# Kernel tuning notes

Measured on AMD Instinct MI355X. Metric: run time of the kernel, lower is better.

## Reference

```python
import math
import jax, jax.numpy as jnp
import numpy as np

B, S, DIM = 1, 1024, 2048
H, KVH, HD = 16, 4, 128
HID, L, VOCAB = 8192, 2, 32000
NIMG, TOK_START = 256, 1
IMG_IN = 2 * 14 * 14 * 3  # temporal_patch*spatial_patch^2*channels
EPS = 1e-6


def _rms(x, w=None, eps=EPS):
    y = x * jax.lax.rsqrt(jnp.mean(x * x, axis=-1, keepdims=True) + eps)
    return y if w is None else y * w


def _rope(x, angles):
    # x: [B,S,H,D], angles: [S, D//2] pairwise rotation angles (3D RoPE: 1D+2D concat)
    c = jnp.cos(angles)[None, :, None, :]
    s = jnp.sin(angles)[None, :, None, :]
    x1, x2 = x[..., 0::2], x[..., 1::2]
    return jnp.stack([x1 * c - x2 * s, x1 * s + x2 * c], axis=-1).reshape(x.shape)


def setup_inputs() -> dict:
    key = jax.random.key(0)
    ks = jax.random.split(key, 12)
    sc = 0.02
    return {
        "tokens": jax.random.randint(ks[0], (B, S), 0, VOCAB),
        "img_feats": jax.random.normal(ks[1], (B, NIMG, IMG_IN), jnp.float32),
        "freqs_cis": jax.random.normal(ks[2], (S, HD // 4), jnp.float32),
        "freqs_cis_2d": jax.random.normal(ks[3], (S, HD // 4), jnp.float32),
        "tok_emb": jax.random.normal(ks[4], (VOCAB, DIM), jnp.float32) * sc,
        "img_proj_w": jax.random.normal(ks[5], (DIM, IMG_IN), jnp.float32) * sc,
        "wqkv": jax.random.normal(ks[6], (L, H * HD + 2 * KVH * HD, DIM), jnp.float32) * sc,
        "wo": jax.random.normal(ks[7], (L, DIM, H * HD), jnp.float32) * sc,
        "sinks": jax.random.normal(ks[8], (L, H), jnp.float32),
        "w13": jax.random.normal(ks[9], (L, 2 * HID, DIM), jnp.float32) * sc,
        "w2": jax.random.normal(ks[10], (L, DIM, HID), jnp.float32) * sc,
        "norm_w": jnp.ones((DIM,), jnp.float32),
        "output_w": jax.random.normal(ks[11], (VOCAB, DIM), jnp.float32) * sc,
    }


def reference(tokens, img_feats, freqs_cis, freqs_cis_2d, tok_emb, img_proj_w,
              wqkv, wo, sinks, w13, w2, norm_w, output_w):
    # token embeddings + slice-based scatter of projected image tokens
    x = tok_emb[tokens]                                   # [B,S,DIM]
    img = jnp.einsum('bnf,df->bnd', img_feats, img_proj_w)
    x = jax.lax.dynamic_update_slice(x, img, (0, TOK_START, 0))

    angles = jnp.concatenate([freqs_cis, freqs_cis_2d], axis=-1)  # [S, HD//2]
    scale = 1.0 / math.sqrt(HD)
    neg = jnp.where(jnp.tril(jnp.ones((S, S), bool)), 0.0, -jnp.inf)  # causal
    n_rep = H // KVH
    q_dim, kv_dim = H * HD, KVH * HD

    for i in range(L):
        # attention: RMSNorm -> QKV -> QK-norm -> GQA expand -> RoPE -> SDPA+lse
        h = _rms(x)
        qkv = h @ wqkv[i].T
        q = qkv[..., :q_dim].reshape(B, S, H, HD)
        k = qkv[..., q_dim:q_dim + kv_dim].reshape(B, S, KVH, HD)
        v = qkv[..., q_dim + kv_dim:].reshape(B, S, KVH, HD)
        q, k = _rms(q), _rms(k)
        k = jnp.repeat(k, n_rep, axis=2)  # repeat_interleave over kv heads
        v = jnp.repeat(v, n_rep, axis=2)
        q, k = _rope(q, angles), _rope(k, angles)
        scores = jnp.einsum('bqhd,bkhd->bhqk', q, k) * scale + neg
        lse = jax.nn.logsumexp(scores, axis=-1)            # [B,H,S]
        attn = jnp.exp(scores - lse[..., None])
        out = jnp.einsum('bhqk,bkhd->bqhd', attn, v)        # [B,S,H,HD]
        sink_scale = jax.nn.sigmoid(lse - sinks[i][None, :, None])  # [B,H,S]
        out = out * sink_scale.transpose(0, 2, 1)[..., None]
        x = x + out.reshape(B, S, H * HD) @ wo[i].T

        # FFN: RMSNorm -> interleaved gate/up -> relu(gate)^2 * up -> down
        h = _rms(x)
        packed = h @ w13[i].T
        gate, up = packed[..., 0::2], packed[..., 1::2]
        x = x + (jnp.square(jax.nn.relu(gate)) * up) @ w2[i].T

    return _rms(x, norm_w) @ output_w.T                    # [B,S,VOCAB]
```

## Files before the change

kernel.cpp:

```cpp
#include <hip/hip_runtime.h>

typedef __bf16 bf16;
typedef bf16 bf16x8 __attribute__((ext_vector_type(8)));
typedef bf16 bf16x4 __attribute__((ext_vector_type(4)));
typedef bf16 bf16x2 __attribute__((ext_vector_type(2)));
typedef float f32x4 __attribute__((ext_vector_type(4)));
typedef float f32x2 __attribute__((ext_vector_type(2)));

#define S_LEN 1024
#define DIM 2048
#define NH 16
#define NKVH 4
#define HD 128
#define HID 8192
#define VOCAB 32000
#define QKV_N 3072
#define W13_N 16384
#define IMG_K 1176
#define NIMG 256

#define AS1 __attribute__((address_space(1)))
#define AS3 __attribute__((address_space(3)))

__device__ inline f32x4 mfma16(bf16x8 a, bf16x8 b, f32x4 c) {
  return __builtin_amdgcn_mfma_f32_16x16x32_bf16(a, b, c, 0, 0, 0);
}

__global__ void embed_kernel(const int* __restrict__ tok, const float* __restrict__ emb,
                             float* __restrict__ x) {
  int s = blockIdx.x, t = threadIdx.x;
  int id = tok[s];
  const float* er = emb + (size_t)id * DIM;
  float* xr = x + (size_t)s * DIM;
  *(f32x4*)(xr + t * 8)     = *(const f32x4*)(er + t * 8);
  *(f32x4*)(xr + t * 8 + 4) = *(const f32x4*)(er + t * 8 + 4);
}

__global__ void cvt_kernel(const float* __restrict__ in, bf16* __restrict__ o, int n) {
  int i = blockIdx.x * 256 + threadIdx.x;
  if (i < n) o[i] = (bf16)in[i];
}
__global__ void cvt4_kernel(const float* __restrict__ in, bf16* __restrict__ o, int n4) {
  int i = blockIdx.x * 256 + threadIdx.x;
  if (i < n4) {
    f32x4 v = *(const f32x4*)(in + (size_t)i * 4);
    bf16x4 b;
    b[0] = (bf16)v[0]; b[1] = (bf16)v[1]; b[2] = (bf16)v[2]; b[3] = (bf16)v[3];
    *(bf16x4*)(o + (size_t)i * 4) = b;
  }
}

template<int USE_W>
__global__ void rmsnorm_kernel(const float* __restrict__ x, const float* __restrict__ w,
                               bf16* __restrict__ o) {
  const int row = blockIdx.x, t = threadIdx.x;
  const float* xr = x + (size_t)row * DIM;
  f32x4 a = *(const f32x4*)(xr + t * 8);
  f32x4 b = *(const f32x4*)(xr + t * 8 + 4);
  float ss = a[0]*a[0] + a[1]*a[1] + a[2]*a[2] + a[3]*a[3]
           + b[0]*b[0] + b[1]*b[1] + b[2]*b[2] + b[3]*b[3];
#pragma unroll
  for (int off = 1; off < 64; off <<= 1) ss += __shfl_xor(ss, off);
  __shared__ float red[4];
  if ((t & 63) == 0) red[t >> 6] = ss;
  __syncthreads();
  ss = red[0] + red[1] + red[2] + red[3];
  float r = rsqrtf(ss * (1.0f / DIM) + 1e-6f);
  bf16x8 ov;
  if (USE_W) {
    f32x4 w1 = *(const f32x4*)(w + t * 8);
    f32x4 w2v = *(const f32x4*)(w + t * 8 + 4);
    ov[0] = (bf16)(a[0]*r*w1[0]); ov[1] = (bf16)(a[1]*r*w1[1]);
    ov[2] = (bf16)(a[2]*r*w1[2]); ov[3] = (bf16)(a[3]*r*w1[3]);
    ov[4] = (bf16)(b[0]*r*w2v[0]); ov[5] = (bf16)(b[1]*r*w2v[1]);
    ov[6] = (bf16)(b[2]*r*w2v[2]); ov[7] = (bf16)(b[3]*r*w2v[3]);
  } else {
    ov[0] = (bf16)(a[0]*r); ov[1] = (bf16)(a[1]*r);
    ov[2] = (bf16)(a[2]*r); ov[3] = (bf16)(a[3]*r);
    ov[4] = (bf16)(b[0]*r); ov[5] = (bf16)(b[1]*r);
    ov[6] = (bf16)(b[2]*r); ov[7] = (bf16)(b[3]*r);
  }
  *(bf16x8*)(o + (size_t)row * DIM + t * 8) = ov;
}

__global__ void qkvpost_kernel(const float* __restrict__ qkv, const float* __restrict__ f1,
                               const float* __restrict__ f2, bf16* __restrict__ qb,
                               bf16* __restrict__ kb, bf16* __restrict__ vtb) {
  int s = blockIdx.x, t = threadIdx.x;
  __shared__ float cs[64], sn[64];
  if (t < 64) {
    float ang = (t < 32) ? f1[(size_t)s * 32 + t] : f2[(size_t)s * 32 + (t - 32)];
    cs[t] = cosf(ang);
    sn[t] = sinf(ang);
  }
  __syncthreads();
  int w = t >> 6, lane = t & 63;
  for (int hh = w; hh < 24; hh += 4) {
    const float* base = qkv + (size_t)s * QKV_N + hh * HD;
    f32x2 e = *(const f32x2*)(base + lane * 2);
    if (hh < 20) {
      float ssum = e[0]*e[0] + e[1]*e[1];
#pragma unroll
      for (int off = 1; off < 64; off <<= 1) ssum += __shfl_xor(ssum, off);
      float r = rsqrtf(ssum * (1.0f / HD) + 1e-6f);
      float x1 = e[0] * r, x2 = e[1] * r;
      float c = cs[lane], s2 = sn[lane];
      bf16x2 ov;
      ov[0] = (bf16)(x1 * c - x2 * s2);
      ov[1] = (bf16)(x1 * s2 + x2 * c);
      if (hh < 16)
        *(bf16x2*)(qb + ((size_t)hh * S_LEN + s) * HD + lane * 2) = ov;
      else
        *(bf16x2*)(kb + ((size_t)(hh - 16) * S_LEN + s) * HD + lane * 2) = ov;
    } else {
      int kv = hh - 20;
      vtb[((size_t)kv * HD + lane * 2) * S_LEN + s]     = (bf16)e[0];
      vtb[((size_t)kv * HD + lane * 2 + 1) * S_LEN + s] = (bf16)e[1];
    }
  }
}

__global__ __launch_bounds__(256) void attn_kernel(const bf16* __restrict__ qb,
                                                   const bf16* __restrict__ kb,
                                                   const bf16* __restrict__ vtb,
                                                   const float* __restrict__ sinks,
                                                   bf16* __restrict__ out) {
  const int h = blockIdx.y, qs = blockIdx.x;
  const int w = threadIdx.x >> 6, lane = threadIdx.x & 63;
  const int lo = lane & 15, hi = lane >> 4;
  const int q0 = qs * 16;
  const int q = q0 + lo;
  const int kvh = h >> 2;
  const bf16* Q = qb + (size_t)h * S_LEN * HD;
  const bf16* Kp = kb + (size_t)kvh * S_LEN * HD;
  const bf16* Vt = vtb + (size_t)kvh * HD * S_LEN;
  const float scale = 0.08838834764831845f;

  __shared__ float accS[4][64 * 36];
  __shared__ float mS[4][16], lS[4][16];

  bf16x8 qf[4];
#pragma unroll
  for (int ks = 0; ks < 4; ++ks)
    qf[ks] = *(const bf16x8*)(Q + (size_t)q * HD + ks * 32 + hi * 8);

  f32x4 accT[8];
#pragma unroll
  for (int i = 0; i < 8; ++i) accT[i] = (f32x4){0.f, 0.f, 0.f, 0.f};
  float mrow = -3e38f, lrow = 0.f;

  const int ntc = (q0 + 15) / 64 + 1;
  for (int c = w; c < ntc; c += 4) {
    const int kv0 = c * 64;
    f32x4 st[4];
#pragma unroll
    for (int f = 0; f < 4; ++f) st[f] = (f32x4){0.f, 0.f, 0.f, 0.f};
#pragma unroll
    for (int ks = 0; ks < 4; ++ks) {
      const bf16* kbase = Kp + (size_t)(kv0 + lo) * HD + ks * 32 + hi * 8;
#pragma unroll
      for (int f = 0; f < 4; ++f) {
        bf16x8 kf = *(const bf16x8*)(kbase + (size_t)f * 16 * HD);
        st[f] = mfma16(kf, qf[ks], st[f]);
      }
    }
    float p[4][4];
    float pmax = -3e38f;
#pragma unroll
    for (int f = 0; f < 4; ++f)
#pragma unroll
      for (int r = 0; r < 4; ++r) {
        int kvg = kv0 + f * 16 + hi * 4 + r;
        float v = (kvg <= q) ? st[f][r] * scale : -3e38f;
        p[f][r] = v;
        pmax = fmaxf(pmax, v);
      }
    pmax = fmaxf(pmax, __shfl_xor(pmax, 16));
    pmax = fmaxf(pmax, __shfl_xor(pmax, 32));
    float mnew = fmaxf(mrow, pmax);
    float alpha = __expf(mrow - mnew);
    float ps = 0.f;
#pragma unroll
    for (int f = 0; f < 4; ++f)
#pragma unroll
      for (int r = 0; r < 4; ++r) {
        float e = __expf(p[f][r] - mnew);
        p[f][r] = e;
        ps += e;
      }
    ps += __shfl_xor(ps, 16);
    ps += __shfl_xor(ps, 32);
    lrow = lrow * alpha + ps;
    mrow = mnew;
#pragma unroll
    for (int fd = 0; fd < 8; ++fd) {
      accT[fd][0] *= alpha; accT[fd][1] *= alpha;
      accT[fd][2] *= alpha; accT[fd][3] *= alpha;
    }
    bf16x8 pb0, pb1;
#pragma unroll
    for (int j = 0; j < 8; ++j) {
      int src = ((j >> 2) + 2 * (hi & 1)) * 16 + lo;
      float v0 = __shfl(p[0][j & 3], src);
      float v1 = __shfl(p[1][j & 3], src);
      pb0[j] = (bf16)((hi >= 2) ? v1 : v0);
      float v2 = __shfl(p[2][j & 3], src);
      float v3 = __shfl(p[3][j & 3], src);
      pb1[j] = (bf16)((hi >= 2) ? v3 : v2);
    }
#pragma unroll
    for (int fd = 0; fd < 8; ++fd) {
      const bf16* vrow = Vt + (size_t)(fd * 16 + lo) * S_LEN + kv0 + hi * 8;
      bf16x8 vf0 = *(const bf16x8*)(vrow);
      bf16x8 vf1 = *(const bf16x8*)(vrow + 32);
      accT[fd] = mfma16(vf0, pb0, accT[fd]);
      accT[fd] = mfma16(vf1, pb1, accT[fd]);
    }
  }
  if (hi == 0) { mS[w][lo] = mrow; lS[w][lo] = lrow; }
  float* as = &accS[w][lane * 36];
#pragma unroll
  for (int fd = 0; fd < 8; ++fd) *(f32x4*)(as + fd * 4) = accT[fd];
  __syncthreads();
  float m0 = mS[0][lo], m1 = mS[1][lo], m2 = mS[2][lo], m3 = mS[3][lo];
  float mstar = fmaxf(fmaxf(m0, m1), fmaxf(m2, m3));
  float e0 = __expf(m0 - mstar), e1 = __expf(m1 - mstar);
  float e2 = __expf(m2 - mstar), e3 = __expf(m3 - mstar);
  float lstar = lS[0][lo]*e0 + lS[1][lo]*e1 + lS[2][lo]*e2 + lS[3][lo]*e3;
  float lse = mstar + __logf(lstar);
  float ssig = 1.f / (1.f + __expf(sinks[h] - lse));
  float sc = ssig / lstar;
#pragma unroll
  for (int f2 = 0; f2 < 2; ++f2) {
    int fd = w * 2 + f2;
    f32x4 a0 = *(const f32x4*)&accS[0][lane * 36 + fd * 4];
    f32x4 a1 = *(const f32x4*)&accS[1][lane * 36 + fd * 4];
    f32x4 a2 = *(const f32x4*)&accS[2][lane * 36 + fd * 4];
    f32x4 a3 = *(const f32x4*)&accS[3][lane * 36 + fd * 4];
#pragma unroll
    for (int r = 0; r < 4; ++r) {
      float o = a0[r]*e0 + a1[r]*e1 + a2[r]*e2 + a3[r]*e3;
      out[(size_t)q * DIM + h * HD + fd * 16 + hi * 4 + r] = (bf16)(o * sc);
    }
  }
}

__device__ inline void xcd_remap(int ntm, int ntn, int& mtile, int& ntile) {
  const int flat = blockIdx.x + ntm * blockIdx.y;
  const int chunk = ntm * 8;
  const int gfull = ntn >> 3;
  const int g = flat / chunk;
  if (g < gfull) {
    int rem = flat - g * chunk;
    ntile = g * 8 + (rem & 7);
    mtile = rem >> 3;
  } else {
    int rem = flat - gfull * chunk;
    int nrem = ntn - gfull * 8;
    ntile = gfull * 8 + rem % nrem;
    mtile = rem / nrem;
  }
}

enum { EPI_STORE = 0, EPI_ADD = 1, EPI_ACT = 2, EPI_ADDA = 3 };

template<int BM, int BN, int EPI, int GL>
__global__ void gemm_bt(const bf16* __restrict__ A, const float* __restrict__ W,
                        float* __restrict__ C, bf16* __restrict__ Cb,
                        int M, int N, int K, int ldc) {
  constexpr int BK = 64;
  __shared__ __align__(16) char lds[(BM + BN) * BK * 2];
  char* ldsA = lds;
  char* ldsB = lds + BM * BK * 2;
  const int t = threadIdx.x;
  int mtile, ntile;
  xcd_remap(gridDim.x, gridDim.y, mtile, ntile);
  const int m0 = mtile * BM, n0 = ntile * BN;

  const int wid = t >> 6, lane = t & 63;
  const int lo = lane & 15, hi = lane >> 4;
  const int wr = wid >> 1, wc = wid & 1;
  constexpr int TM = BM / 32, TN = BN / 32;
  constexpr int NA = BM / 32;
  constexpr int NPASS = BM / 32;
  constexpr int NW = BN / 16;

  f32x4 acc[TM][TN];
#pragma unroll
  for (int m = 0; m < TM; ++m)
#pragma unroll
    for (int n = 0; n < TN; ++n) acc[m][n] = (f32x4){0.f, 0.f, 0.f, 0.f};

  const int nk = (K + BK - 1) / BK;
  for (int kt = 0; kt < nk; ++kt) {
    const int k0 = kt * BK;
    bf16x8 av[NA];
    f32x4 wv[NW];
    if (!GL) {
#pragma unroll
      for (int i = 0; i < NA; ++i) {
        int c = t + i * 256;
        int row = c >> 3, kc = c & 7;
        int kg = k0 + kc * 8;
        bf16x8 z = {};
        av[i] = (kg < K) ? *(const bf16x8*)(A + (size_t)(m0 + row) * K + kg) : z;
      }
    }
#pragma unroll
    for (int i = 0; i < NW; ++i) {
      int c = t + i * 256;
      int row = c >> 4, kc = c & 15;
      int kg = k0 + kc * 4;
      f32x4 z = (f32x4){0.f, 0.f, 0.f, 0.f};
      wv[i] = (kg < K) ? *(const f32x4*)(W + (size_t)(n0 + row) * K + kg) : z;
    }
    __syncthreads();
    if (GL) {
#pragma unroll
      for (int i = 0; i < NPASS; ++i) {
        int row = i * 32 + (t >> 3);
        int srcb = ((t & 7) * 16) ^ ((row & 7) << 4);
        const bf16* g2 = A + (size_t)(m0 + row) * K + k0 + (srcb >> 1);
        char* l = ldsA + i * 4096 + wid * 1024;
        __builtin_amdgcn_global_load_lds((const AS1 void*)g2, (AS3 void*)l, 16, 0, 0);
      }
    } else {
#pragma unroll
      for (int i = 0; i < NA; ++i) {
        int c = t + i * 256;
        int row = c >> 3, kc = c & 7;
        int kb = (kc * 16) ^ ((row & 7) << 4);
        *(bf16x8*)(ldsA + row * 128 + kb) = av[i];
      }
    }
#pragma unroll
    for (int i = 0; i < NW; ++i) {
      int c = t + i * 256;
      int row = c >> 4, kc = c & 15;
      bf16x4 bv;
      bv[0] = (bf16)wv[i][0]; bv[1] = (bf16)wv[i][1];
      bv[2] = (bf16)wv[i][2]; bv[3] = (bf16)wv[i][3];
      int kb = (kc * 8) ^ ((row & 7) << 4);
      *(bf16x4*)(ldsB + row * 128 + kb) = bv;
    }
    __syncthreads();
#pragma unroll
    for (int ks = 0; ks < 2; ++ks) {
      bf16x8 af[TM], bfr[TN];
      int kbb = ks * 64 + hi * 16;
#pragma unroll
      for (int m = 0; m < TM; ++m) {
        int row = wr * (BM / 2) + m * 16 + lo;
        af[m] = *(const bf16x8*)(ldsA + row * 128 + (kbb ^ ((row & 7) << 4)));
      }
#pragma unroll
      for (int n = 0; n < TN; ++n) {
        int row = wc * (BN / 2) + n * 16 + lo;
        bfr[n] = *(const bf16x8*)(ldsB + row * 128 + (kbb ^ ((row & 7) << 4)));
      }
#pragma unroll
      for (int m = 0; m < TM; ++m)
#pragma unroll
        for (int n = 0; n < TN; ++n)
          acc[m][n] = mfma16(af[m], bfr[n], acc[m][n]);
    }
    __syncthreads();
  }
#pragma unroll
  for (int m = 0; m < TM; ++m) {
    int gmb = m0 + wr * (BM / 2) + m * 16 + hi * 4;
#pragma unroll
    for (int n = 0; n < TN; ++n) {
      int gn = n0 + wc * (BN / 2) + n * 16 + lo;
#pragma unroll
      for (int r = 0; r < 4; ++r) {
        float v = acc[m][n][r];
        if (EPI == EPI_STORE) {
          C[(size_t)(gmb + r) * ldc + gn] = v;
        } else if (EPI == EPI_ADD) {
          C[(size_t)(gmb + r) * ldc + gn] += v;
        } else {
          float pv = __shfl_xor(v, 1);
          if (!(lane & 1)) {
            float g2 = fmaxf(v, 0.f);
            Cb[(size_t)(gmb + r) * (W13_N / 2) + (gn >> 1)] = (bf16)(g2 * g2 * pv);
          }
        }
      }
    }
  }
}

template<int BM, int BN, int EPI>
__global__ __launch_bounds__(256) void gemm_bb(const bf16* __restrict__ A,
                                               const bf16* __restrict__ W,
                                               float* __restrict__ C, bf16* __restrict__ Cb,
                                               int strideK, int kLen, int ldc) {
  constexpr int BK = 64;
  __shared__ __align__(16) char lds[(BM + BN) * BK * 2];
  char* ldsA = lds;
  char* ldsB = lds + BM * BK * 2;
  const int t = threadIdx.x;
  int mtile, ntile;
  xcd_remap(gridDim.x, gridDim.y, mtile, ntile);
  const int m0 = mtile * BM, n0 = ntile * BN;
  const int koff = blockIdx.z * kLen;

  const int wid = t >> 6, lane = t & 63;
  const int lo = lane & 15, hi = lane >> 4;
  const int wr = wid >> 1, wc = wid & 1;
  constexpr int TM = BM / 32, TN = BN / 32;
  constexpr int PA = BM / 32, PB = BN / 32;

  f32x4 acc[TM][TN];
#pragma unroll
  for (int m = 0; m < TM; ++m)
#pragma unroll
    for (int n = 0; n < TN; ++n) acc[m][n] = (f32x4){0.f, 0.f, 0.f, 0.f};

  const int prow = t >> 3;
  const int psrcb = (t & 7) * 16;
  const int nk = kLen / BK;
  for (int kt = 0; kt < nk; ++kt) {
    const int k0 = koff + kt * BK;
#pragma unroll
    for (int i = 0; i < PA; ++i) {
      int row = i * 32 + prow;
      int srcb = psrcb ^ ((row & 7) << 4);
      const bf16* g = A + (size_t)(m0 + row) * strideK + k0 + (srcb >> 1);
      __builtin_amdgcn_global_load_lds((const AS1 void*)g,
                                       (AS3 void*)(ldsA + i * 4096 + wid * 1024), 16, 0, 0);
    }
#pragma unroll
    for (int i = 0; i < PB; ++i) {
      int row = i * 32 + prow;
      int srcb = psrcb ^ ((row & 7) << 4);
      const bf16* g = W + (size_t)(n0 + row) * strideK + k0 + (srcb >> 1);
      __builtin_amdgcn_global_load_lds((const AS1 void*)g,
                                       (AS3 void*)(ldsB + i * 4096 + wid * 1024), 16, 0, 0);
    }
    __syncthreads();
#pragma unroll
    for (int ks = 0; ks < 2; ++ks) {
      bf16x8 af[TM], bfr[TN];
      int kbb = ks * 64 + hi * 16;
#pragma unroll
      for (int m = 0; m < TM; ++m) {
        int row = wr * (BM / 2) + m * 16 + lo;
        af[m] = *(const bf16x8*)(ldsA + row * 128 + (kbb ^ ((row & 7) << 4)));
      }
#pragma unroll
      for (int n = 0; n < TN; ++n) {
        int row = wc * (BN / 2) + n * 16 + lo;
        bfr[n] = *(const bf16x8*)(ldsB + row * 128 + (kbb ^ ((row & 7) << 4)));
      }
#pragma unroll
      for (int m = 0; m < TM; ++m)
#pragma unroll
        for (int n = 0; n < TN; ++n)
          acc[m][n] = mfma16(af[m], bfr[n], acc[m][n]);
    }
    __syncthreads();
  }
#pragma unroll
  for (int m = 0; m < TM; ++m) {
    int gmb = m0 + wr * (BM / 2) + m * 16 + hi * 4;
#pragma unroll
    for (int n = 0; n < TN; ++n) {
      int gn = n0 + wc * (BN / 2) + n * 16 + lo;
#pragma unroll
      for (int r = 0; r < 4; ++r) {
        float v = acc[m][n][r];
        if (EPI == EPI_STORE) {
          C[(size_t)(gmb + r) * ldc + gn] = v;
        } else if (EPI == EPI_ADD) {
          C[(size_t)(gmb + r) * ldc + gn] += v;
        } else if (EPI == EPI_ADDA) {
          atomicAdd(&C[(size_t)(gmb + r) * ldc + gn], v);
        } else {
          float pv = __shfl_xor(v, 1);
          if (!(lane & 1)) {
            float g2 = fmaxf(v, 0.f);
            Cb[(size_t)(gmb + r) * (W13_N / 2) + (gn >> 1)] = (bf16)(g2 * g2 * pv);
          }
        }
      }
    }
  }
}

template<int EPI>
__global__ __launch_bounds__(512, 1) void gemm_2pf(const bf16* __restrict__ A,
                                                   const float* __restrict__ W,
                                                   float* __restrict__ C, bf16* __restrict__ Cb,
                                                   int K, int ldc) {
  extern __shared__ __align__(16) char lds[];
  char* ldsA = lds;
  char* ldsB = lds + 65536;
  const int t = threadIdx.x;
  int mtile, ntile;
  xcd_remap(gridDim.x, gridDim.y, mtile, ntile);
  const int m0 = mtile * 256, n0 = ntile * 256;
  const int wid = t >> 6, lane = t & 63;
  const int lo = lane & 15, hi = lane >> 4;
  const int wr = wid >> 2, wc = wid & 3;

  f32x4 acc[8][4];
#pragma unroll
  for (int f = 0; f < 8; ++f)
#pragma unroll
    for (int g = 0; g < 4; ++g) acc[f][g] = (f32x4){0.f, 0.f, 0.f, 0.f};

  const int prow = t >> 3;
  const int pcol = (t & 7) * 16;

  auto STAGEA = [&](int h, int kt2) {
    char* dst = ldsA + (kt2 & 1) * 32768 + h * 16384;
    const int k0 = kt2 * 64;
#pragma unroll
    for (int i = 0; i < 2; ++i) {
      int row = i * 64 + prow;
      int srcb = pcol ^ ((row & 7) << 4);
      const bf16* g = A + (size_t)(m0 + h * 128 + row) * K + k0 + (srcb >> 1);
      __builtin_amdgcn_global_load_lds((const AS1 void*)g,
          (AS3 void*)(dst + i * 8192 + wid * 1024), 16, 0, 0);
    }
  };

  f32x4 breg[4][2];
  auto BLOAD = [&](int kt2) {
#pragma unroll
    for (int i = 0; i < 4; ++i) {
      int c = t + i * 512;
      int row = c >> 3, kc = c & 7;
      const float* g = W + (size_t)(n0 + row) * K + kt2 * 64 + kc * 8;
      breg[i][0] = *(const f32x4*)(g);
      breg[i][1] = *(const f32x4*)(g + 4);
    }
  };
  auto BWRITE = [&](int kt2) {
#pragma unroll
    for (int i = 0; i < 4; ++i) {
      int c = t + i * 512;
      int row = c >> 3, kc = c & 7;
      int h = row >> 7, rowh = row & 127;
      bf16x8 bv;
#pragma unroll
      for (int e = 0; e < 4; ++e) {
        bv[e]     = (bf16)breg[i][0][e];
        bv[4 + e] = (bf16)breg[i][1][e];
      }
      *(bf16x8*)(ldsB + (kt2 & 1) * 32768 + h * 16384 + rowh * 128 +
                 ((kc * 16) ^ ((rowh & 7) << 4))) = bv;
    }
  };

  auto LDA = [&](int buf, int mh, int i, int ks) -> bf16x8 {
    int row = (mh * 4 + i) * 16 + lo;
    return *(const bf16x8*)(ldsA + buf * 32768 + wr * 16384 + row * 128 +
                            ((ks * 64 + hi * 16) ^ ((row & 7) << 4)));
  };
  auto LDB = [&](int buf, int nh, int j, int ks) -> bf16x8 {
    int rowh = (wc & 1) * 64 + (nh * 2 + j) * 16 + lo;
    return *(const bf16x8*)(ldsB + buf * 32768 + (wc >> 1) * 16384 + rowh * 128 +
                            ((ks * 64 + hi * 16) ^ ((rowh & 7) << 4)));
  };

  const int nk = K / 64;
  STAGEA(0, 0);
  STAGEA(1, 0);
  __builtin_amdgcn_sched_barrier(0);
  BLOAD(0);
  __builtin_amdgcn_sched_barrier(0);
  asm volatile("s_waitcnt vmcnt(8)" ::: "memory");
  __builtin_amdgcn_s_barrier();
  asm volatile("" ::: "memory");

  for (int kt = 0; kt < nk; ++kt) {
    const int buf = kt & 1;
    const bool more = (kt + 1) < nk;
    BWRITE(kt);
    asm volatile("s_waitcnt lgkmcnt(0)" ::: "memory");
    __builtin_amdgcn_s_barrier();
    asm volatile("" ::: "memory");
    if (more) {
      STAGEA(0, kt + 1);
      STAGEA(1, kt + 1);
      __builtin_amdgcn_sched_barrier(0);
      BLOAD(kt + 1);
      __builtin_amdgcn_sched_barrier(0);
    }
#pragma unroll
    for (int mh = 0; mh < 2; ++mh) {
      bf16x8 a[4][2];
#pragma unroll
      for (int i = 0; i < 4; ++i) { a[i][0] = LDA(buf, mh, i, 0); a[i][1] = LDA(buf, mh, i, 1); }
#pragma unroll
      for (int nh = 0; nh < 2; ++nh) {
        bf16x8 b[2][2];
#pragma unroll
        for (int j = 0; j < 2; ++j) { b[j][0] = LDB(buf, nh, j, 0); b[j][1] = LDB(buf, nh, j, 1); }
        __builtin_amdgcn_s_setprio(1);
#pragma unroll
        for (int i = 0; i < 4; ++i)
#pragma unroll
          for (int j = 0; j < 2; ++j) {
            acc[mh * 4 + i][nh * 2 + j] = mfma16(a[i][0], b[j][0], acc[mh * 4 + i][nh * 2 + j]);
            acc[mh * 4 + i][nh * 2 + j] = mfma16(a[i][1], b[j][1], acc[mh * 4 + i][nh * 2 + j]);
          }
        __builtin_amdgcn_s_setprio(0);
      }
    }
    if (more) asm volatile("s_waitcnt vmcnt(8)" ::: "memory");
    else      asm volatile("s_waitcnt vmcnt(0)" ::: "memory");
    __builtin_amdgcn_s_barrier();
    asm volatile("" ::: "memory");
  }
#pragma unroll
  for (int f = 0; f < 8; ++f) {
    int gmb = m0 + wr * 128 + f * 16 + hi * 4;
#pragma unroll
    for (int g = 0; g < 4; ++g) {
      int gn = n0 + wc * 64 + g * 16 + lo;
#pragma unroll
      for (int r = 0; r < 4; ++r) {
        float v = acc[f][g][r];
        if (EPI == EPI_STORE) {
          C[(size_t)(gmb + r) * ldc + gn] = v;
        } else if (EPI == EPI_ADD) {
          C[(size_t)(gmb + r) * ldc + gn] += v;
        } else {
          float pv = __shfl_xor(v, 1);
          if (!(lane & 1)) {
            float g2 = fmaxf(v, 0.f);
            Cb[(size_t)(gmb + r) * (W13_N / 2) + (gn >> 1)] = (bf16)(g2 * g2 * pv);
          }
        }
      }
    }
  }
}

extern "C" void kernel_launch(void* const* d_in, const int* in_sizes, int n_in,
                              void* d_out, int out_size, void* d_ws, size_t ws_size,
                              hipStream_t stream) {
  const int* tokens = (const int*)d_in[0];
  const float* img_feats = (const float*)d_in[1];
  const float* freqs = (const float*)d_in[2];
  const float* freqs2 = (const float*)d_in[3];
  const float* tok_emb = (const float*)d_in[4];
  const float* img_proj_w = (const float*)d_in[5];
  const float* wqkv = (const float*)d_in[6];
  const float* wo = (const float*)d_in[7];
  const float* sinks = (const float*)d_in[8];
  const float* w13 = (const float*)d_in[9];
  const float* w2 = (const float*)d_in[10];
  const float* norm_w = (const float*)d_in[11];
  const float* output_w = (const float*)d_in[12];
  float* out = (float*)d_out;

  char* ws = (char*)d_ws;
  float* x = (float*)ws;   ws += (size_t)S_LEN * DIM * 4;
  bf16* h = (bf16*)ws;     ws += (size_t)S_LEN * DIM * 2;
  float* qkv = (float*)ws; ws += (size_t)S_LEN * QKV_N * 4;
  bf16* qb = (bf16*)ws;    ws += (size_t)NH * S_LEN * HD * 2;
  bf16* kb = (bf16*)ws;    ws += (size_t)NKVH * S_LEN * HD * 2;
  bf16* vtb = (bf16*)ws;   ws += (size_t)NKVH * HD * S_LEN * 2;
  bf16* ao = (bf16*)ws;    ws += (size_t)S_LEN * DIM * 2;
  bf16* act = (bf16*)ws;   ws += (size_t)S_LEN * HID * 2;
  bf16* imgb = (bf16*)ws;  ws += (size_t)NIMG * IMG_K * 2;
  const size_t n_wqkv = (size_t)2 * QKV_N * DIM;
  const size_t n_wo   = (size_t)2 * DIM * (NH * HD);
  const size_t n_w2   = (size_t)2 * DIM * HID;
  bf16* wqkvb = (bf16*)ws; ws += n_wqkv * 2;
  bf16* wob   = (bf16*)ws; ws += n_wo * 2;
  bf16* w2b   = (bf16*)ws; ws += n_w2 * 2;
  const bool bf16_path = ((size_t)(ws - (char*)d_ws) <= ws_size);

  bool big_ok = false;
  {
    hipError_t e1 = hipFuncSetAttribute((const void*)&gemm_2pf<EPI_STORE>,
                                        hipFuncAttributeMaxDynamicSharedMemorySize, 131072);
    hipError_t e2 = hipFuncSetAttribute((const void*)&gemm_2pf<EPI_ACT>,
                                        hipFuncAttributeMaxDynamicSharedMemorySize, 131072);
    if (e1 == hipSuccess && e2 == hipSuccess) {
      hipFuncAttributes fa1{}, fa2{};
      if (hipFuncGetAttributes(&fa1, (const void*)&gemm_2pf<EPI_STORE>) == hipSuccess &&
          hipFuncGetAttributes(&fa2, (const void*)&gemm_2pf<EPI_ACT>) == hipSuccess)
        big_ok = fa1.maxDynamicSharedSizeBytes >= 131072 &&
                 fa2.maxDynamicSharedSizeBytes >= 131072;
    }
  }

  embed_kernel<<<S_LEN, 256, 0, stream>>>(tokens, tok_emb, x);
  cvt_kernel<<<(NIMG * IMG_K + 255) / 256, 256, 0, stream>>>(img_feats, imgb, NIMG * IMG_K);
  gemm_bt<64, 128, EPI_STORE, 0><<<dim3(NIMG / 64, DIM / 128), 256, 0, stream>>>(
      imgb, img_proj_w, x + DIM, nullptr, NIMG, DIM, IMG_K, DIM);

  if (bf16_path) {
    cvt4_kernel<<<(int)(n_wqkv / 4 + 255) / 256, 256, 0, stream>>>(wqkv, wqkvb, (int)(n_wqkv / 4));
    cvt4_kernel<<<(int)(n_wo / 4 + 255) / 256, 256, 0, stream>>>(wo, wob, (int)(n_wo / 4));
    cvt4_kernel<<<(int)(n_w2 / 4 + 255) / 256, 256, 0, stream>>>(w2, w2b, (int)(n_w2 / 4));
  }

  for (int i = 0; i < 2; ++i) {
    rmsnorm_kernel<0><<<S_LEN, 256, 0, stream>>>(x, nullptr, h);
    if (bf16_path) {
      gemm_bb<64, 128, EPI_STORE><<<dim3(S_LEN / 64, QKV_N / 128, 1), 256, 0, stream>>>(
          h, wqkvb + (size_t)i * QKV_N * DIM, qkv, nullptr, DIM, DIM, QKV_N);
    } else {
      gemm_bt<64, 128, EPI_STORE, 1><<<dim3(S_LEN / 64, QKV_N / 128), 256, 0, stream>>>(
          h, wqkv + (size_t)i * QKV_N * DIM, qkv, nullptr, S_LEN, QKV_N, DIM, QKV_N);
    }
    qkvpost_kernel<<<S_LEN, 256, 0, stream>>>(qkv, freqs, freqs2, qb, kb, vtb);
    attn_kernel<<<dim3(S_LEN / 16, NH), 256, 0, stream>>>(qb, kb, vtb, sinks + i * NH, ao);
    if (bf16_path) {
      gemm_bb<64, 128, EPI_ADDA><<<dim3(S_LEN / 64, DIM / 128, 2), 256, 0, stream>>>(
          ao, wob + (size_t)i * DIM * DIM, x, nullptr, DIM, DIM / 2, DIM);
    } else {
      gemm_bt<64, 128, EPI_ADD, 1><<<dim3(S_LEN / 64, DIM / 128), 256, 0, stream>>>(
          ao, wo + (size_t)i * DIM * DIM, x, nullptr, S_LEN, DIM, DIM, DIM);
    }
    rmsnorm_kernel<0><<<S_LEN, 256, 0, stream>>>(x, nullptr, h);
    if (big_ok) {
      gemm_2pf<EPI_ACT><<<dim3(S_LEN / 256, W13_N / 256), 512, 131072, stream>>>(
          h, w13 + (size_t)i * W13_N * DIM, nullptr, act, DIM, 0);
    } else {
      gemm_bt<128, 128, EPI_ACT, 1><<<dim3(S_LEN / 128, W13_N / 128), 256, 0, stream>>>(
          h, w13 + (size_t)i * W13_N * DIM, nullptr, act, S_LEN, W13_N, DIM, 0);
    }
    if (bf16_path) {
      gemm_bb<64, 128, EPI_ADDA><<<dim3(S_LEN / 64, DIM / 128, 2), 256, 0, stream>>>(
          act, w2b + (size_t)i * DIM * HID, x, nullptr, HID, HID / 2, DIM);
    } else {
      gemm_bt<64, 128, EPI_ADD, 1><<<dim3(S_LEN / 64, DIM / 128), 256, 0, stream>>>(
          act, w2 + (size_t)i * DIM * HID, x, nullptr, S_LEN, DIM, HID, DIM);
    }
  }
  rmsnorm_kernel<1><<<S_LEN, 256, 0, stream>>>(x, norm_w, h);
  if (big_ok) {
    gemm_2pf<EPI_STORE><<<dim3(S_LEN / 256, VOCAB / 256), 512, 131072, stream>>>(
        h, output_w, out, nullptr, DIM, VOCAB);
  } else {
    gemm_bt<128, 128, EPI_STORE, 1><<<dim3(S_LEN / 128, VOCAB / 128), 256, 0, stream>>>(
        h, output_w, out, nullptr, S_LEN, VOCAB, DIM, VOCAB);
  }
}
```

Before: 894.5 us.

## Load fp32 B fragments directly from global into registers, drop B LDS staging

In the 256x256 gemm_2pf kernel, the B (fp32 weight) tile is no longer loaded into registers, converted, and written to LDS. Each wave now reads its own B fragments straight from global memory, converts them to bf16 in registers, and feeds them to MFMA. This halves dynamic LDS to 64KB and removes one barrier plus the LDS write/read traffic per k-step. In exchange, B loads are no longer prefetched a step ahead and are now on the critical path with a vmcnt(0) wait each iteration. Waves that share columns also reload the same B data, raising global/L2 traffic.

```diff
diff --git a/kernel.cpp b/kernel.cpp
--- a/kernel.cpp
+++ b/kernel.cpp
@@ -496,7 +496,6 @@
                                                    int K, int ldc) {
   extern __shared__ __align__(16) char lds[];
   char* ldsA = lds;
-  char* ldsB = lds + 65536;
   const int t = threadIdx.x;
   int mtile, ntile;
   xcd_remap(gridDim.x, gridDim.y, mtile, ntile);
@@ -527,92 +526,62 @@
     }
   };
 
-  f32x4 breg[4][2];
-  auto BLOAD = [&](int kt2) {
-#pragma unroll
-    for (int i = 0; i < 4; ++i) {
-      int c = t + i * 512;
-      int row = c >> 3, kc = c & 7;
-      const float* g = W + (size_t)(n0 + row) * K + kt2 * 64 + kc * 8;
-      breg[i][0] = *(const f32x4*)(g);
-      breg[i][1] = *(const f32x4*)(g + 4);
-    }
-  };
-  auto BWRITE = [&](int kt2) {
-#pragma unroll
-    for (int i = 0; i < 4; ++i) {
-      int c = t + i * 512;
-      int row = c >> 3, kc = c & 7;
-      int h = row >> 7, rowh = row & 127;
-      bf16x8 bv;
-#pragma unroll
-      for (int e = 0; e < 4; ++e) {
-        bv[e]     = (bf16)breg[i][0][e];
-        bv[4 + e] = (bf16)breg[i][1][e];
-      }
-      *(bf16x8*)(ldsB + (kt2 & 1) * 32768 + h * 16384 + rowh * 128 +
-                 ((kc * 16) ^ ((rowh & 7) << 4))) = bv;
-    }
-  };
-
   auto LDA = [&](int buf, int mh, int i, int ks) -> bf16x8 {
     int row = (mh * 4 + i) * 16 + lo;
     return *(const bf16x8*)(ldsA + buf * 32768 + wr * 16384 + row * 128 +
                             ((ks * 64 + hi * 16) ^ ((row & 7) << 4)));
   };
-  auto LDB = [&](int buf, int nh, int j, int ks) -> bf16x8 {
-    int rowh = (wc & 1) * 64 + (nh * 2 + j) * 16 + lo;
-    return *(const bf16x8*)(ldsB + buf * 32768 + (wc >> 1) * 16384 + rowh * 128 +
-                            ((ks * 64 + hi * 16) ^ ((rowh & 7) << 4)));
+  const int bn_base = n0 + (wc >> 1) * 128 + (wc & 1) * 64;
+  auto BFRAG = [&](int nh, int j, int ks, int kt2) -> bf16x8 {
+    const float* g = W + (size_t)(bn_base + (nh * 2 + j) * 16 + lo) * K +
+                     kt2 * 64 + ks * 32 + hi * 8;
+    f32x4 v0 = *(const f32x4*)(g);
+    f32x4 v1 = *(const f32x4*)(g + 4);
+    bf16x8 b;
+#pragma unroll
+    for (int e = 0; e < 4; ++e) { b[e] = (bf16)v0[e]; b[4 + e] = (bf16)v1[e]; }
+    return b;
   };
 
   const int nk = K / 64;
   STAGEA(0, 0);
   STAGEA(1, 0);
-  __builtin_amdgcn_sched_barrier(0);
-  BLOAD(0);
-  __builtin_amdgcn_sched_barrier(0);
-  asm volatile("s_waitcnt vmcnt(8)" ::: "memory");
+  asm volatile("s_waitcnt vmcnt(0)" ::: "memory");
   __builtin_amdgcn_s_barrier();
   asm volatile("" ::: "memory");
 
   for (int kt = 0; kt < nk; ++kt) {
     const int buf = kt & 1;
     const bool more = (kt + 1) < nk;
-    BWRITE(kt);
-    asm volatile("s_waitcnt lgkmcnt(0)" ::: "memory");
-    __builtin_amdgcn_s_barrier();
-    asm volatile("" ::: "memory");
     if (more) {
       STAGEA(0, kt + 1);
       STAGEA(1, kt + 1);
       __builtin_amdgcn_sched_barrier(0);
-      BLOAD(kt + 1);
-      __builtin_amdgcn_sched_barrier(0);
-    }
+    }
+    bf16x8 b00 = BFRAG(0, 0, 0, kt), b01 = BFRAG(0, 0, 1, kt);
+    bf16x8 b10 = BFRAG(0, 1, 0, kt), b11 = BFRAG(0, 1, 1, kt);
+    bf16x8 b20 = BFRAG(1, 0, 0, kt), b21 = BFRAG(1, 0, 1, kt);
+    bf16x8 b30 = BFRAG(1, 1, 0, kt), b31 = BFRAG(1, 1, 1, kt);
 #pragma unroll
     for (int mh = 0; mh < 2; ++mh) {
       bf16x8 a[4][2];
 #pragma unroll
       for (int i = 0; i < 4; ++i) { a[i][0] = LDA(buf, mh, i, 0); a[i][1] = LDA(buf, mh, i, 1); }
-#pragma unroll
-      for (int nh = 0; nh < 2; ++nh) {
-        bf16x8 b[2][2];
-#pragma unroll
-        for (int j = 0; j < 2; ++j) { b[j][0] = LDB(buf, nh, j, 0); b[j][1] = LDB(buf, nh, j, 1); }
-        __builtin_amdgcn_s_setprio(1);
-#pragma unroll
-        for (int i = 0; i < 4; ++i)
-#pragma unroll
-          for (int j = 0; j < 2; ++j) {
-            acc[mh * 4 + i][nh * 2 + j] = mfma16(a[i][0], b[j][0], acc[mh * 4 + i][nh * 2 + j]);
-            acc[mh * 4 + i][nh * 2 + j] = mfma16(a[i][1], b[j][1], acc[mh * 4 + i][nh * 2 + j]);
-          }
-        __builtin_amdgcn_s_setprio(0);
-      }
-    }
-    if (more) asm volatile("s_waitcnt vmcnt(8)" ::: "memory");
-    else      asm volatile("s_waitcnt vmcnt(0)" ::: "memory");
+      __builtin_amdgcn_s_setprio(1);
+#pragma unroll
+      for (int i = 0; i < 4; ++i) {
+        acc[mh * 4 + i][0] = mfma16(a[i][0], b00, acc[mh * 4 + i][0]);
+        acc[mh * 4 + i][0] = mfma16(a[i][1], b01, acc[mh * 4 + i][0]);
+        acc[mh * 4 + i][1] = mfma16(a[i][0], b10, acc[mh * 4 + i][1]);
+        acc[mh * 4 + i][1] = mfma16(a[i][1], b11, acc[mh * 4 + i][1]);
+        acc[mh * 4 + i][2] = mfma16(a[i][0], b20, acc[mh * 4 + i][2]);
+        acc[mh * 4 + i][2] = mfma16(a[i][1], b21, acc[mh * 4 + i][2]);
+        acc[mh * 4 + i][3] = mfma16(a[i][0], b30, acc[mh * 4 + i][3]);
+        acc[mh * 4 + i][3] = mfma16(a[i][1], b31, acc[mh * 4 + i][3]);
+      }
+      __builtin_amdgcn_s_setprio(0);
+    }
+    asm volatile("s_waitcnt vmcnt(0)" ::: "memory");
     __builtin_amdgcn_s_barrier();
     asm volatile("" ::: "memory");
   }
@@ -621,7 +590,7 @@
     int gmb = m0 + wr * 128 + f * 16 + hi * 4;
 #pragma unroll
     for (int g = 0; g < 4; ++g) {
-      int gn = n0 + wc * 64 + g * 16 + lo;
+      int gn = bn_base + g * 16 + lo;
 #pragma unroll
       for (int r = 0; r < 4; ++r) {
         float v = acc[f][g][r];
@@ -680,15 +649,15 @@
   bool big_ok = false;
   {
     hipError_t e1 = hipFuncSetAttribute((const void*)&gemm_2pf<EPI_STORE>,
-                                        hipFuncAttributeMaxDynamicSharedMemorySize, 131072);
+                                        hipFuncAttributeMaxDynamicSharedMemorySize, 65536);
     hipError_t e2 = hipFuncSetAttribute((const void*)&gemm_2pf<EPI_ACT>,
-                                        hipFuncAttributeMaxDynamicSharedMemorySize, 131072);
+                                        hipFuncAttributeMaxDynamicSharedMemorySize, 65536);
     if (e1 == hipSuccess && e2 == hipSuccess) {
       hipFuncAttributes fa1{}, fa2{};
       if (hipFuncGetAttributes(&fa1, (const void*)&gemm_2pf<EPI_STORE>) == hipSuccess &&
           hipFuncGetAttributes(&fa2, (const void*)&gemm_2pf<EPI_ACT>) == hipSuccess)
-        big_ok = fa1.maxDynamicSharedSizeBytes >= 131072 &&
-                 fa2.maxDynamicSharedSizeBytes >= 131072;
+        big_ok = fa1.maxDynamicSharedSizeBytes >= 65536 &&
+                 fa2.maxDynamicSharedSizeBytes >= 65536;
     }
   }
 
@@ -723,7 +692,7 @@
     }
     rmsnorm_kernel<0><<<S_LEN, 256, 0, stream>>>(x, nullptr, h);
     if (big_ok) {
-      gemm_2pf<EPI_ACT><<<dim3(S_LEN / 256, W13_N / 256), 512, 131072, stream>>>(
+      gemm_2pf<EPI_ACT><<<dim3(S_LEN / 256, W13_N / 256), 512, 65536, stream>>>(
           h, w13 + (size_t)i * W13_N * DIM, nullptr, act, DIM, 0);
     } else {
       gemm_bt<128, 128, EPI_ACT, 1><<<dim3(S_LEN / 128, W13_N / 128), 256, 0, stream>>>(
@@ -739,7 +708,7 @@
   }
   rmsnorm_kernel<1><<<S_LEN, 256, 0, stream>>>(x, norm_w, h);
   if (big_ok) {
-    gemm_2pf<EPI_STORE><<<dim3(S_LEN / 256, VOCAB / 256), 512, 131072, stream>>>(
+    gemm_2pf<EPI_STORE><<<dim3(S_LEN / 256, VOCAB / 256), 512, 65536, stream>>>(
         h, output_w, out, nullptr, DIM, VOCAB);
   } else {
     gemm_bt<128, 128, EPI_STORE, 1><<<dim3(S_LEN / 128, VOCAB / 128), 256, 0, stream>>>(
```

Measured after the change: 1.232 ms. +37.7%, slower.
